# Optimization experiments

Hardware: AMD Instinct MI355X
Metric: run time of the kernel (lower is better)

The kernel has to match this reference:

```python
import jax, jax.numpy as jnp
import numpy as np

S, B, C, H = 384, 2, 768, 12
CC = C // H

def setup_inputs() -> dict:
    key = jax.random.key(0)
    ks = jax.random.split(key, 8)
    x = jax.random.normal(ks[0], (S, B, C), dtype=jnp.float32)
    pe = jax.random.normal(ks[1], (S, S, B, C), dtype=jnp.float32)
    # causal mask: True where key index t > query index s (masked out)
    cm = (jnp.arange(S)[None, :] > jnp.arange(S)[:, None])[:, :, None]
    cm = jnp.broadcast_to(cm, (S, S, B))
    pm = jnp.zeros((S, S, B), dtype=bool)  # unused by the module's forward
    stdv = 1.0 / C ** 0.5
    qkv_w = jax.random.normal(ks[2], (3 * C, C), dtype=jnp.float32) * stdv
    qkv_b = jax.random.normal(ks[3], (3 * C,), dtype=jnp.float32) * stdv
    u = jax.random.uniform(ks[4], (C,), minval=-stdv, maxval=stdv, dtype=jnp.float32)
    w = jax.random.uniform(ks[5], (C,), minval=-stdv, maxval=stdv, dtype=jnp.float32)
    out_w = jax.random.normal(ks[6], (C, C), dtype=jnp.float32) * stdv
    out_b = jax.random.normal(ks[7], (C,), dtype=jnp.float32) * stdv
    return {"x": x, "pe": pe, "cm": cm, "pm": pm, "qkv_w": qkv_w,
            "qkv_b": qkv_b, "u": u, "w": w, "out_w": out_w, "out_b": out_b}

def reference(x, pe, cm, pm, qkv_w, qkv_b, u, w, out_w, out_b):
    s, b, c = x.shape
    qkv = x @ qkv_w.T + qkv_b                       # (s,b,3c)
    q, k, v = jnp.split(qkv, 3, axis=-1)
    q = q.reshape(s, b, H, CC)
    k = k.reshape(s, b, H, CC)
    v = v.reshape(s, b, H, CC)
    uh = u.reshape(1, 1, H, CC)
    wh = w.reshape(1, 1, H, CC)
    # content-content scores with global content bias u
    dd_ud = jnp.einsum('sbhc,tbhc->stbh', q + uh, k)
    # content-position scores against dense pairwise pe
    pe5 = pe.reshape(s, s, b, H, CC)
    dp_wp = jnp.einsum('sbhc,stbhc->stbh', q + wh, pe5)
    scale = 1.0 / CC ** 0.5
    a = (dd_ud + dp_wp) * scale
    a = jnp.where(cm[..., None], -jnp.inf, a)       # causal mask (intended)
    p = jax.nn.softmax(a, axis=1)                   # softmax over key axis t
    o = jnp.einsum('stbh,tbhc->sbhc', p, v).reshape(s, b, c)
    return o @ out_w.T + out_b
```

## Files before the change

kernel.cpp:

```cpp
#include <hip/hip_runtime.h>
#include <hip/hip_bf16.h>
#include <cstdint>

constexpr int kS  = 384;
constexpr int kB  = 2;
constexpr int kC  = 768;
constexpr int kH  = 12;
constexpr int kCC = 64;
constexpr int kHPB = 4;

typedef __attribute__((ext_vector_type(8))) short short8;
typedef __attribute__((ext_vector_type(4))) float f32x4;
typedef __attribute__((ext_vector_type(4))) unsigned short u16x4;
typedef const __attribute__((address_space(1))) unsigned int glb_u32_t;
typedef __attribute__((address_space(3))) unsigned int lds_u32_t;

static __device__ __forceinline__ ushort f2bf(float f) {
  __hip_bfloat16 h = __float2bfloat16(f);
  return *reinterpret_cast<ushort*>(&h);
}
static __device__ __forceinline__ float bf2f(ushort x) {
  unsigned v = (unsigned)x << 16;
  return __builtin_bit_cast(float, v);
}

template <int CTRL>
static __device__ __forceinline__ float dpp_add(float x) {
  int xi = __builtin_bit_cast(int, x);
  int yi = __builtin_amdgcn_update_dpp(0, xi, CTRL, 0xF, 0xF, true);
  return x + __builtin_bit_cast(float, yi);
}
static __device__ __forceinline__ float row16_sum(float x) {
  x = dpp_add<0xB1>(x);
  x = dpp_add<0x4E>(x);
  x = dpp_add<0x124>(x);
  x = dpp_add<0x128>(x);
  return x;
}

__global__ __launch_bounds__(256) void convert_bf16(
    const float* __restrict__ x, const float* __restrict__ qw,
    const float* __restrict__ ow, ushort* __restrict__ xb,
    ushort* __restrict__ qwb, ushort* __restrict__ owb) {
  int idx = blockIdx.x * 256 + threadIdx.x;
  const float* src;
  ushort* dst;
  if (idx < 147456) {
    src = x; dst = xb;
  } else if (idx < 147456 + 442368) {
    idx -= 147456; src = qw; dst = qwb;
  } else {
    idx -= 589824; src = ow; dst = owb;
  }
  f32x4 v = *reinterpret_cast<const f32x4*>(src + (size_t)idx * 4);
  u16x4 o;
  o[0] = f2bf(v[0]); o[1] = f2bf(v[1]); o[2] = f2bf(v[2]); o[3] = f2bf(v[3]);
  *reinterpret_cast<u16x4*>(dst + (size_t)idx * 4) = o;
}

__global__ __launch_bounds__(256) void gemm_qkv(
    const ushort* __restrict__ Abf, const ushort* __restrict__ Wbf,
    const float* __restrict__ bias, float* __restrict__ qbuf,
    ushort* __restrict__ kbuf, ushort* __restrict__ vbuf, int K) {
  __shared__ ushort As[64 * 64];
  __shared__ ushort Ws[64 * 64];
  const int tid = threadIdx.x;
  const int m0 = blockIdx.y * 64, n0 = blockIdx.x * 64;
  const int wv = tid >> 6, l = tid & 63;
  const int wr = wv >> 1, wc = wv & 1;
  const int lr = l & 15, lk = l >> 4;

  f32x4 acc[2][2] = {{{0.f, 0.f, 0.f, 0.f}, {0.f, 0.f, 0.f, 0.f}},
                     {{0.f, 0.f, 0.f, 0.f}, {0.f, 0.f, 0.f, 0.f}}};

  for (int k0 = 0; k0 < K; k0 += 64) {
    __syncthreads();
#pragma unroll
    for (int j = 0; j < 2; ++j) {
      int cid = (j * 4 + wv) * 64 + l;
      int r = cid >> 3, c = cid & 7;
      int cs = c ^ (r & 7);
      const ushort* ga = Abf + (size_t)(m0 + r) * K + k0 + cs * 8;
      __builtin_amdgcn_global_load_lds((glb_u32_t*)ga,
                                       (lds_u32_t*)&As[(cid & ~63) * 8],
                                       16, 0, 0);
      const ushort* gw = Wbf + (size_t)(n0 + r) * K + k0 + cs * 8;
      __builtin_amdgcn_global_load_lds((glb_u32_t*)gw,
                                       (lds_u32_t*)&Ws[(cid & ~63) * 8],
                                       16, 0, 0);
    }
    __syncthreads();
#pragma unroll
    for (int ks = 0; ks < 2; ++ks) {
      short8 af[2], bw[2];
#pragma unroll
      for (int f = 0; f < 2; ++f) {
        int ra = wr * 32 + f * 16 + lr;
        int ca = (ks * 4 + lk) ^ (ra & 7);
        af[f] = *reinterpret_cast<const short8*>(&As[(ra * 8 + ca) * 8]);
        int rb = wc * 32 + f * 16 + lr;
        int cb = (ks * 4 + lk) ^ (rb & 7);
        bw[f] = *reinterpret_cast<const short8*>(&Ws[(rb * 8 + cb) * 8]);
      }
#pragma unroll
      for (int fr = 0; fr < 2; ++fr)
#pragma unroll
        for (int fc = 0; fc < 2; ++fc)
          acc[fr][fc] = __builtin_amdgcn_mfma_f32_16x16x32_bf16(
              af[fr], bw[fc], acc[fr][fc], 0, 0, 0);
    }
  }

  const int seg = n0 / kC;
  const int nc0 = n0 - seg * kC;
#pragma unroll
  for (int fr = 0; fr < 2; ++fr)
#pragma unroll
    for (int fc = 0; fc < 2; ++fc)
#pragma unroll
      for (int j = 0; j < 4; ++j) {
        int m = m0 + wr * 32 + fr * 16 + lk * 4 + j;
        int n = nc0 + wc * 32 + fc * 16 + lr;
        float val = acc[fr][fc][j] + bias[seg * kC + n];
        if (seg == 0) {
          qbuf[(size_t)m * kC + n] = val;
        } else {
          int t = m >> 1, bb = m & 1;
          ushort* dst = (seg == 1) ? kbuf : vbuf;
          dst[((size_t)bb * kS + t) * kC + n] = f2bf(val);
        }
      }
}

__global__ __launch_bounds__(256) void gemm_bf16_lds(
    const ushort* __restrict__ Abf, const ushort* __restrict__ Wbf,
    const float* __restrict__ bias, float* __restrict__ Cg,
    int M, int N, int K) {
  __shared__ ushort As[64 * 64];
  __shared__ ushort Ws[64 * 64];
  const int tid = threadIdx.x;
  const int m0 = blockIdx.y * 64, n0 = blockIdx.x * 64;
  const int wv = tid >> 6, l = tid & 63;
  const int wr = wv >> 1, wc = wv & 1;
  const int lr = l & 15, lk = l >> 4;

  f32x4 acc[2][2] = {{{0.f, 0.f, 0.f, 0.f}, {0.f, 0.f, 0.f, 0.f}},
                     {{0.f, 0.f, 0.f, 0.f}, {0.f, 0.f, 0.f, 0.f}}};

  for (int k0 = 0; k0 < K; k0 += 64) {
    __syncthreads();
#pragma unroll
    for (int j = 0; j < 2; ++j) {
      int cid = (j * 4 + wv) * 64 + l;
      int r = cid >> 3, c = cid & 7;
      int cs = c ^ (r & 7);
      const ushort* ga = Abf + (size_t)(m0 + r) * K + k0 + cs * 8;
      __builtin_amdgcn_global_load_lds((glb_u32_t*)ga,
                                       (lds_u32_t*)&As[(cid & ~63) * 8],
                                       16, 0, 0);
      const ushort* gw = Wbf + (size_t)(n0 + r) * K + k0 + cs * 8;
      __builtin_amdgcn_global_load_lds((glb_u32_t*)gw,
                                       (lds_u32_t*)&Ws[(cid & ~63) * 8],
                                       16, 0, 0);
    }
    __syncthreads();
#pragma unroll
    for (int ks = 0; ks < 2; ++ks) {
      short8 af[2], bw[2];
#pragma unroll
      for (int f = 0; f < 2; ++f) {
        int ra = wr * 32 + f * 16 + lr;
        int ca = (ks * 4 + lk) ^ (ra & 7);
        af[f] = *reinterpret_cast<const short8*>(&As[(ra * 8 + ca) * 8]);
        int rb = wc * 32 + f * 16 + lr;
        int cb = (ks * 4 + lk) ^ (rb & 7);
        bw[f] = *reinterpret_cast<const short8*>(&Ws[(rb * 8 + cb) * 8]);
      }
#pragma unroll
      for (int fr = 0; fr < 2; ++fr)
#pragma unroll
        for (int fc = 0; fc < 2; ++fc)
          acc[fr][fc] = __builtin_amdgcn_mfma_f32_16x16x32_bf16(
              af[fr], bw[fc], acc[fr][fc], 0, 0, 0);
    }
  }

#pragma unroll
  for (int fr = 0; fr < 2; ++fr)
#pragma unroll
    for (int fc = 0; fc < 2; ++fc)
#pragma unroll
      for (int j = 0; j < 4; ++j) {
        int m = m0 + wr * 32 + fr * 16 + lk * 4 + j;
        int n = n0 + wc * 32 + fc * 16 + lr;
        Cg[(size_t)m * N + n] = acc[fr][fc][j] + bias[n];
      }
}

__global__ __launch_bounds__(256, 6) void attn_kernel(
    const float* __restrict__ qbuf, const float* __restrict__ pe,
    const ushort* __restrict__ kb, const ushort* __restrict__ vb,
    const float* __restrict__ u, const float* __restrict__ w,
    ushort* __restrict__ obf) {
  __shared__ float sc[kHPB][kS];

  const int bid = blockIdx.x;
  const int sb = bid / (kH / kHPB);
  const int hg = bid % (kH / kHPB);
  const int s = kS - 1 - (sb >> 1);
  const int b = sb & 1;
  const int wave = threadIdx.x >> 6;
  const int h = hg * kHPB + wave;
  const int lane = threadIdx.x & 63;
  const int tq = lane >> 4;
  const int cq = (lane & 15) * 4;
  const int ch = h * kCC + cq;
  const float scale = 0.125f;

  const int row = s * kB + b;
  const f32x4 q4 = *(const f32x4*)&qbuf[(size_t)row * kC + ch];
  const f32x4 u4 = *(const f32x4*)&u[ch];
  const f32x4 w4 = *(const f32x4*)&w[ch];
  const f32x4 qu = q4 + u4;
  const f32x4 qw = q4 + w4;

  const ushort* kbase = kb + ((size_t)b * kS) * kC + ch;
  const ushort* vbase = vb + ((size_t)b * kS) * kC + ch;
  const float* pbase = pe + ((int64_t)s * kS * kB + b) * kC + ch;
  const int pstride = kB * kC;

  const int nfull = (s + 1) & ~15;

  int t0 = 0;
  for (; t0 < nfull; t0 += 16) {
    f32x4 p4[4];
    u16x4 kd[4];
#pragma unroll
    for (int i = 0; i < 4; ++i) {
      int t = t0 + i * 4 + tq;
      p4[i] = __builtin_nontemporal_load(
          (const f32x4*)&pbase[(int64_t)t * pstride]);
      kd[i] = *(const u16x4*)&kbase[(size_t)t * kC];
    }
#pragma unroll
    for (int i = 0; i < 4; ++i) {
      float r = qu[0] * bf2f(kd[i][0]) + qu[1] * bf2f(kd[i][1]) +
                qu[2] * bf2f(kd[i][2]) + qu[3] * bf2f(kd[i][3]) +
                qw[0] * p4[i][0] + qw[1] * p4[i][1] +
                qw[2] * p4[i][2] + qw[3] * p4[i][3];
      r = row16_sum(r);
      if ((lane & 15) == 0) sc[wave][t0 + i * 4 + tq] = r * scale;
    }
  }
  for (; t0 <= s; t0 += 4) {
    int t = t0 + tq;
    int tc = (t <= s) ? t : s;
    f32x4 p4 = __builtin_nontemporal_load(
        (const f32x4*)&pbase[(int64_t)tc * pstride]);
    u16x4 kd = *(const u16x4*)&kbase[(size_t)tc * kC];
    float r = qu[0] * bf2f(kd[0]) + qu[1] * bf2f(kd[1]) +
              qu[2] * bf2f(kd[2]) + qu[3] * bf2f(kd[3]) +
              qw[0] * p4[0] + qw[1] * p4[1] + qw[2] * p4[2] + qw[3] * p4[3];
    r = row16_sum(r);
    if ((lane & 15) == 0 && t <= s) sc[wave][t] = r * scale;
  }
  __syncthreads();

  float mx = -1e30f;
  for (int t = lane; t <= s; t += 64) mx = fmaxf(mx, sc[wave][t]);
#pragma unroll
  for (int off = 32; off; off >>= 1) mx = fmaxf(mx, __shfl_xor(mx, off, 64));
  float sum = 0.f;
  for (int t = lane; t <= s; t += 64) {
    float e = __expf(sc[wave][t] - mx);
    sc[wave][t] = e;
    sum += e;
  }
#pragma unroll
  for (int off = 32; off; off >>= 1) sum += __shfl_xor(sum, off, 64);
  const float rden = 1.0f / sum;

  f32x4 oa = {0.f, 0.f, 0.f, 0.f};
  t0 = 0;
  for (; t0 < nfull; t0 += 16) {
    u16x4 vd[4];
    float p[4];
#pragma unroll
    for (int i = 0; i < 4; ++i) {
      int t = t0 + i * 4 + tq;
      vd[i] = *(const u16x4*)&vbase[(size_t)t * kC];
      p[i] = sc[wave][t];
    }
#pragma unroll
    for (int i = 0; i < 4; ++i) {
      oa[0] += p[i] * bf2f(vd[i][0]); oa[1] += p[i] * bf2f(vd[i][1]);
      oa[2] += p[i] * bf2f(vd[i][2]); oa[3] += p[i] * bf2f(vd[i][3]);
    }
  }
  for (; t0 <= s; t0 += 4) {
    int t = t0 + tq;
    if (t <= s) {
      float p = sc[wave][t];
      u16x4 vd = *(const u16x4*)&vbase[(size_t)t * kC];
      oa[0] += p * bf2f(vd[0]); oa[1] += p * bf2f(vd[1]);
      oa[2] += p * bf2f(vd[2]); oa[3] += p * bf2f(vd[3]);
    }
  }
#pragma unroll
  for (int off = 16; off <= 32; off <<= 1) {
    oa[0] += __shfl_xor(oa[0], off);
    oa[1] += __shfl_xor(oa[1], off);
    oa[2] += __shfl_xor(oa[2], off);
    oa[3] += __shfl_xor(oa[3], off);
  }
  if (lane < 16) {
    u16x4 res;
    res[0] = f2bf(oa[0] * rden); res[1] = f2bf(oa[1] * rden);
    res[2] = f2bf(oa[2] * rden); res[3] = f2bf(oa[3] * rden);
    *reinterpret_cast<u16x4*>(&obf[(int64_t)row * kC + ch]) = res;
  }
}

extern "C" void kernel_launch(void* const* d_in, const int* in_sizes, int n_in,
                              void* d_out, int out_size, void* d_ws,
                              size_t ws_size, hipStream_t stream) {
  const float* x     = (const float*)d_in[0];
  const float* pe    = (const float*)d_in[1];
  const float* qkv_w = (const float*)d_in[4];
  const float* qkv_b = (const float*)d_in[5];
  const float* u     = (const float*)d_in[6];
  const float* w     = (const float*)d_in[7];
  const float* out_w = (const float*)d_in[8];
  const float* out_b = (const float*)d_in[9];
  float* out = (float*)d_out;

  char* wsb = (char*)d_ws;
  float*  qbuf = (float*)wsb;
  ushort* xb   = (ushort*)(wsb + 2359296);
  ushort* qwb  = (ushort*)(wsb + 3538944);
  ushort* owb  = (ushort*)(wsb + 7077888);
  ushort* obf  = (ushort*)(wsb + 8257536);
  ushort* kbuf = (ushort*)(wsb + 9437184);
  ushort* vbuf = (ushort*)(wsb + 10616832);

  convert_bf16<<<2880, 256, 0, stream>>>(x, qkv_w, out_w, xb, qwb, owb);

  gemm_qkv<<<dim3(3 * kC / 64, kS * kB / 64), 256, 0, stream>>>(
      xb, qwb, qkv_b, qbuf, kbuf, vbuf, kC);

  attn_kernel<<<kS * kB * (kH / kHPB), kHPB * 64, 0, stream>>>(
      qbuf, pe, kbuf, vbuf, u, w, obf);

  gemm_bf16_lds<<<dim3(kC / 64, kS * kB / 64), 256, 0, stream>>>(
      obf, owb, out_b, out, kS * kB, kC, kC);
}
```

Baseline: 120.7 us.

## Precompute content-content scores with a separate MFMA GEMM kernel

```diff
diff --git a/kernel.cpp b/kernel.cpp
--- a/kernel.cpp
+++ b/kernel.cpp
@@ -60,7 +60,8 @@
 
 __global__ __launch_bounds__(256) void gemm_qkv(
     const ushort* __restrict__ Abf, const ushort* __restrict__ Wbf,
-    const float* __restrict__ bias, float* __restrict__ qbuf,
+    const float* __restrict__ bias, const float* __restrict__ u,
+    float* __restrict__ qbuf, ushort* __restrict__ quB,
     ushort* __restrict__ kbuf, ushort* __restrict__ vbuf, int K) {
   __shared__ ushort As[64 * 64];
   __shared__ ushort Ws[64 * 64];
@@ -124,11 +125,79 @@
         float val = acc[fr][fc][j] + bias[seg * kC + n];
         if (seg == 0) {
           qbuf[(size_t)m * kC + n] = val;
+          quB[(size_t)m * kC + n] = f2bf(val + u[n]);
         } else {
           int t = m >> 1, bb = m & 1;
           ushort* dst = (seg == 1) ? kbuf : vbuf;
           dst[((size_t)bb * kS + t) * kC + n] = f2bf(val);
         }
+      }
+}
+
+__global__ __launch_bounds__(256) void dd_gemm(
+    const ushort* __restrict__ quB, const ushort* __restrict__ kbuf,
+    ushort* __restrict__ dd) {
+  const int tt = blockIdx.x, st = blockIdx.y, bh = blockIdx.z;
+  if (tt > st) return;
+  const int b = bh / kH, h = bh % kH;
+
+  __shared__ ushort Aq[64 * 64];
+  __shared__ ushort Bk[64 * 64];
+  const int tid = threadIdx.x;
+  const int wv = tid >> 6, l = tid & 63;
+  const int wr = wv >> 1, wc = wv & 1;
+  const int lr = l & 15, lk = l >> 4;
+
+#pragma unroll
+  for (int j = 0; j < 2; ++j) {
+    int cid = (j * 4 + wv) * 64 + l;
+    int r = cid >> 3, c = cid & 7;
+    int cs = c ^ (r & 7);
+    const ushort* ga =
+        quB + (size_t)((st * 64 + r) * kB + b) * kC + h * kCC + cs * 8;
+    __builtin_amdgcn_global_load_lds((glb_u32_t*)ga,
+                                     (lds_u32_t*)&Aq[(cid & ~63) * 8],
+                                     16, 0, 0);
+    const ushort* gk =
+        kbuf + ((size_t)b * kS + tt * 64 + r) * kC + h * kCC + cs * 8;
+    __builtin_amdgcn_global_load_lds((glb_u32_t*)gk,
+                                     (lds_u32_t*)&Bk[(cid & ~63) * 8],
+                                     16, 0, 0);
+  }
+  __syncthreads();
+
+  f32x4 acc[2][2] = {{{0.f, 0.f, 0.f, 0.f}, {0.f, 0.f, 0.f, 0.f}},
+                     {{0.f, 0.f, 0.f, 0.f}, {0.f, 0.f, 0.f, 0.f}}};
+#pragma unroll
+  for (int ks = 0; ks < 2; ++ks) {
+    short8 af[2], bw[2];
+#pragma unroll
+    for (int f = 0; f < 2; ++f) {
+      int ra = wr * 32 + f * 16 + lr;
+      int ca = (ks * 4 + lk) ^ (ra & 7);
+      af[f] = *reinterpret_cast<const short8*>(&Aq[(ra * 8 + ca) * 8]);
+      int rb = wc * 32 + f * 16 + lr;
+      int cb = (ks * 4 + lk) ^ (rb & 7);
+      bw[f] = *reinterpret_cast<const short8*>(&Bk[(rb * 8 + cb) * 8]);
+    }
+#pragma unroll
+    for (int fr = 0; fr < 2; ++fr)
+#pragma unroll
+      for (int fc = 0; fc < 2; ++fc)
+        acc[fr][fc] = __builtin_amdgcn_mfma_f32_16x16x32_bf16(
+            af[fr], bw[fc], acc[fr][fc], 0, 0, 0);
+  }
+
+  ushort* drow = dd + (size_t)bh * kS * kS;
+#pragma unroll
+  for (int fr = 0; fr < 2; ++fr)
+#pragma unroll
+    for (int fc = 0; fc < 2; ++fc)
+#pragma unroll
+      for (int j = 0; j < 4; ++j) {
+        int s = st * 64 + wr * 32 + fr * 16 + lk * 4 + j;
+        int t = tt * 64 + wc * 32 + fc * 16 + lr;
+        drow[(size_t)s * kS + t] = f2bf(acc[fr][fc][j]);
       }
 }
 
@@ -199,9 +268,8 @@
 
 __global__ __launch_bounds__(256, 6) void attn_kernel(
     const float* __restrict__ qbuf, const float* __restrict__ pe,
-    const ushort* __restrict__ kb, const ushort* __restrict__ vb,
-    const float* __restrict__ u, const float* __restrict__ w,
-    ushort* __restrict__ obf) {
+    const ushort* __restrict__ dd, const ushort* __restrict__ vb,
+    const float* __restrict__ w, ushort* __restrict__ obf) {
   __shared__ float sc[kHPB][kS];
 
   const int bid = blockIdx.x;
@@ -219,13 +287,11 @@
 
   const int row = s * kB + b;
   const f32x4 q4 = *(const f32x4*)&qbuf[(size_t)row * kC + ch];
-  const f32x4 u4 = *(const f32x4*)&u[ch];
   const f32x4 w4 = *(const f32x4*)&w[ch];
-  const f32x4 qu = q4 + u4;
   const f32x4 qw = q4 + w4;
 
-  const ushort* kbase = kb + ((size_t)b * kS) * kC + ch;
   const ushort* vbase = vb + ((size_t)b * kS) * kC + ch;
+  const ushort* ddrow = dd + ((size_t)(b * kH + h) * kS + s) * kS;
   const float* pbase = pe + ((int64_t)s * kS * kB + b) * kC + ch;
   const int pstride = kB * kC;
 
@@ -234,22 +300,19 @@
   int t0 = 0;
   for (; t0 < nfull; t0 += 16) {
     f32x4 p4[4];
-    u16x4 kd[4];
 #pragma unroll
     for (int i = 0; i < 4; ++i) {
       int t = t0 + i * 4 + tq;
       p4[i] = __builtin_nontemporal_load(
           (const f32x4*)&pbase[(int64_t)t * pstride]);
-      kd[i] = *(const u16x4*)&kbase[(size_t)t * kC];
     }
 #pragma unroll
     for (int i = 0; i < 4; ++i) {
-      float r = qu[0] * bf2f(kd[i][0]) + qu[1] * bf2f(kd[i][1]) +
-                qu[2] * bf2f(kd[i][2]) + qu[3] * bf2f(kd[i][3]) +
-                qw[0] * p4[i][0] + qw[1] * p4[i][1] +
+      int t = t0 + i * 4 + tq;
+      float r = qw[0] * p4[i][0] + qw[1] * p4[i][1] +
                 qw[2] * p4[i][2] + qw[3] * p4[i][3];
       r = row16_sum(r);
-      if ((lane & 15) == 0) sc[wave][t0 + i * 4 + tq] = r * scale;
+      if ((lane & 15) == 0) sc[wave][t] = (r + bf2f(ddrow[t])) * scale;
     }
   }
   for (; t0 <= s; t0 += 4) {
@@ -257,12 +320,10 @@
     int tc = (t <= s) ? t : s;
     f32x4 p4 = __builtin_nontemporal_load(
         (const f32x4*)&pbase[(int64_t)tc * pstride]);
-    u16x4 kd = *(const u16x4*)&kbase[(size_t)tc * kC];
-    float r = qu[0] * bf2f(kd[0]) + qu[1] * bf2f(kd[1]) +
-              qu[2] * bf2f(kd[2]) + qu[3] * bf2f(kd[3]) +
-              qw[0] * p4[0] + qw[1] * p4[1] + qw[2] * p4[2] + qw[3] * p4[3];
+    float r = qw[0] * p4[0] + qw[1] * p4[1] + qw[2] * p4[2] + qw[3] * p4[3];
     r = row16_sum(r);
-    if ((lane & 15) == 0 && t <= s) sc[wave][t] = r * scale;
+    if ((lane & 15) == 0 && t <= s)
+      sc[wave][t] = (r + bf2f(ddrow[t])) * scale;
   }
   __syncthreads();
 
@@ -317,7 +378,7 @@
     u16x4 res;
     res[0] = f2bf(oa[0] * rden); res[1] = f2bf(oa[1] * rden);
     res[2] = f2bf(oa[2] * rden); res[3] = f2bf(oa[3] * rden);
-    *reinterpret_cast<u16x4*>(&obf[(int64_t)row * kC + ch]) = res;
+    *reinterpret_cast<u16x4*>(&obf[(size_t)row * kC + ch]) = res;
   }
 }
 
@@ -336,20 +397,25 @@
 
   char* wsb = (char*)d_ws;
   float*  qbuf = (float*)wsb;
-  ushort* xb   = (ushort*)(wsb + 2359296);
-  ushort* qwb  = (ushort*)(wsb + 3538944);
-  ushort* owb  = (ushort*)(wsb + 7077888);
-  ushort* obf  = (ushort*)(wsb + 8257536);
-  ushort* kbuf = (ushort*)(wsb + 9437184);
-  ushort* vbuf = (ushort*)(wsb + 10616832);
+  ushort* owb  = (ushort*)(wsb + 2359296);
+  ushort* obf  = (ushort*)(wsb + 3538944);
+  ushort* kbuf = (ushort*)(wsb + 4718592);
+  ushort* vbuf = (ushort*)(wsb + 5898240);
+  ushort* quB  = (ushort*)(wsb + 7077888);
+  ushort* xb   = (ushort*)(wsb + 8257536);
+  ushort* qwb  = (ushort*)(wsb + 9437184);
+  ushort* ddb  = (ushort*)(wsb + 8257536);
 
   convert_bf16<<<2880, 256, 0, stream>>>(x, qkv_w, out_w, xb, qwb, owb);
 
   gemm_qkv<<<dim3(3 * kC / 64, kS * kB / 64), 256, 0, stream>>>(
-      xb, qwb, qkv_b, qbuf, kbuf, vbuf, kC);
+      xb, qwb, qkv_b, u, qbuf, quB, kbuf, vbuf, kC);
+
+  dd_gemm<<<dim3(kS / 64, kS / 64, kB * kH), 256, 0, stream>>>(
+      quB, kbuf, ddb);
 
   attn_kernel<<<kS * kB * (kH / kHPB), kHPB * 64, 0, stream>>>(
-      qbuf, pe, kbuf, vbuf, u, w, obf);
+      qbuf, pe, ddb, vbuf, w, obf);
 
   gemm_bf16_lds<<<dim3(kC / 64, kS * kB / 64), 256, 0, stream>>>(
       obf, owb, out_b, out, kS * kB, kC, kC);
```

New measurement: 135.7 us. 12.4% more time.
